# Performance work log

Hardware: AMD Instinct MI355X
Metric: run time of the kernel (lower is better)

Reference implementation:

```python
import jax, jax.numpy as jnp
import numpy as np

S, N, M, D, O = 16, 4096, 128, 128, 128


def setup_inputs() -> dict:
    key = jax.random.key(0)
    kF, kU, kmu, klp, keps = jax.random.split(key, 5)
    return {
        "F": jax.random.normal(kF, (S, N, D), jnp.float32),
        "U": jax.random.normal(kU, (S, M, D), jnp.float32),
        "pseud_mu": jax.random.normal(kmu, (O, M), jnp.float32),
        "pseud_logprec": 0.1 * jax.random.normal(klp, (O, M), jnp.float32),
        "eps": jax.random.normal(keps, (S, O, D), jnp.float32),
    }


def reference(F, U, pseud_mu, pseud_logprec, eps):
    # F: [S,N,D], U: [S,M,D], pseud_mu/pseud_logprec: [O,M], eps: [S,O,D]
    Dd = U.shape[-1]
    phiU = jax.nn.relu(U)                                   # [S,M,D]
    Lp = jnp.exp(pseud_logprec)                             # diag of pseudo precision, [O,M]
    # U^T diag(Lp) U and U^T diag(Lp) v, fused (no dense [M,M] diag, no [S,O,D,M] temp)
    UTLU = jnp.einsum("smd,om,sme->sode", phiU, Lp, phiU)   # [S,O,D,D]
    UTLv = jnp.einsum("smd,om->sod", phiU, Lp * pseud_mu)   # [S,O,D]
    # prior precision = exp(-logvar_p) = I (logvar_p is a fixed zero buffer)
    q_prec = UTLU + jnp.eye(Dd, dtype=UTLU.dtype)           # [S,O,D,D]
    Lc = jnp.linalg.cholesky(q_prec)                        # [S,O,D,D]
    eye = jnp.broadcast_to(jnp.eye(Dd, dtype=q_prec.dtype), q_prec.shape)
    Linv = jax.scipy.linalg.solve_triangular(Lc, eye, lower=True)
    # cholesky_inverse: q_cov = (L L^T)^{-1} = L^{-T} L^{-1}
    q_cov = jnp.einsum("soki,sokj->soij", Linv, Linv)       # [S,O,D,D]
    q_mu = jnp.einsum("sode,soe->sod", q_cov, UTLv)         # [S,O,D]
    # MVN rsample: w = mu + chol(cov) @ eps
    Lcov = jnp.linalg.cholesky(q_cov)                       # [S,O,D,D]
    w = q_mu + jnp.einsum("sode,soe->sod", Lcov, eps)       # [S,O,D]
    # KL(q || N(0, I)) per (s,o), summed over output dim -> [S]
    logdet_cov = 2.0 * jnp.sum(jnp.log(jnp.diagonal(Lcov, axis1=-2, axis2=-1)), axis=-1)
    tr_cov = jnp.trace(q_cov, axis1=-2, axis2=-1)
    kl = 0.5 * (tr_cov + jnp.sum(q_mu * q_mu, axis=-1) - Dd - logdet_cov)  # [S,O]
    kl = jnp.sum(kl, axis=-1)                               # [S]
    F_out = jnp.einsum("sod,snd->sno", w, jax.nn.relu(F))   # [S,N,O]
    U_out = jnp.einsum("sod,smd->smo", w, phiU)             # [S,M,O]
    return F_out, U_out, kl
```

## Files before the change

### kernel.cpp

```cpp
#include <hip/hip_runtime.h>

typedef unsigned int uint;
typedef unsigned short ushort;
typedef __attribute__((ext_vector_type(8))) short b16x8;
typedef __attribute__((ext_vector_type(4))) float f32x4;

#define PHIUT_OFF 0u
#define SQLP_OFF  524288u
#define SMU_OFF   (524288u + 65536u)
#define WBUF_OFF  (524288u + 131072u)
#define KLSO_OFF  (524288u + 131072u + 1048576u)

__device__ __forceinline__ ushort f2bf(float x){
  union { float f; uint u; } v; v.f = x;
  uint r = v.u + 0x7fffu + ((v.u >> 16) & 1u);
  return (ushort)(r >> 16);
}
__device__ __forceinline__ float bflo(uint u){ union { uint uu; float f; } v; v.uu = u << 16; return v.f; }
__device__ __forceinline__ float bfhi(uint u){ union { uint uu; float f; } v; v.uu = u & 0xffff0000u; return v.f; }
__device__ __forceinline__ uint pk2(float a, float b){ return (uint)f2bf(a) | ((uint)f2bf(b) << 16); }
__device__ __forceinline__ float rdl(float x, int l){
  union { float f; int i; } u; u.f = x;
  u.i = __builtin_amdgcn_readlane(u.i, l);
  return u.f;
}

__device__ __forceinline__ void mfma128(const ushort (*A)[136], const ushort (*B)[136],
                                        f32x4 acc[2][8], int wv, int lane){
  const int lr = lane & 15, lk = lane >> 4;
  #pragma unroll
  for (int ti = 0; ti < 2; ++ti)
    #pragma unroll
    for (int tj = 0; tj < 8; ++tj)
      acc[ti][tj] = (f32x4){0.f, 0.f, 0.f, 0.f};
  #pragma unroll
  for (int kk = 0; kk < 4; ++kk){
    const int kof = kk * 32 + lk * 8;
    b16x8 a0 = *(const b16x8*)&A[(wv * 2 + 0) * 16 + lr][kof];
    b16x8 a1 = *(const b16x8*)&A[(wv * 2 + 1) * 16 + lr][kof];
    #pragma unroll
    for (int tj = 0; tj < 8; ++tj){
      b16x8 bf = *(const b16x8*)&B[tj * 16 + lr][kof];
      acc[0][tj] = __builtin_amdgcn_mfma_f32_16x16x32_bf16(a0, bf, acc[0][tj], 0, 0, 0);
      acc[1][tj] = __builtin_amdgcn_mfma_f32_16x16x32_bf16(a1, bf, acc[1][tj], 0, 0, 0);
    }
  }
}

__global__ void k0_prep(const float* __restrict__ U, const float* __restrict__ mu,
                        const float* __restrict__ lp, ushort* __restrict__ phiUT,
                        float* __restrict__ sqlp, float* __restrict__ smu)
{
  __shared__ __align__(16) ushort T0[128][132];
  const int tid = threadIdx.x;
  const int bid = blockIdx.x;
  if (bid < 16){
    const float* Us = U + ((size_t)bid << 14);
    for (int e = tid * 4; e < 16384; e += 1024){
      f32x4 v = *(const f32x4*)&Us[e];
      int m = e >> 7, d = e & 127;
      uint2 pv; pv.x = pk2(fmaxf(v[0],0.f), fmaxf(v[1],0.f));
      pv.y = pk2(fmaxf(v[2],0.f), fmaxf(v[3],0.f));
      *(uint2*)&T0[m][d] = pv;
    }
    __syncthreads();
    ushort* op = phiUT + ((size_t)bid << 14);
    for (int e = tid; e < 16384; e += 256){
      int d = e >> 7, m2 = e & 127;
      op[e] = T0[m2][d];
    }
  } else {
    int idx = ((bid - 16) << 8) + tid;
    float l = lp[idx], m = mu[idx];
    float ex = expf(0.5f * l);
    sqlp[idx] = ex;
    smu[idx]  = ex * m;
  }
}

#define UPJ(J, T) { \
  float s0_=rdl(ya##J[0],(T)), s1_=rdl(ya##J[1],(T)), s2_=rdl(ya##J[2],(T)), s3_=rdl(ya##J[3],(T)); \
  ya##J[0] -= m0_*s0_; ya##J[1] -= m0_*s1_; ya##J[2] -= m0_*s2_; ya##J[3] -= m0_*s3_; \
  yb##J[0] -= m1_*s0_; yb##J[1] -= m1_*s1_; yb##J[2] -= m1_*s2_; yb##J[3] -= m1_*s3_; }

#define UPP0(P,T) { float s1_=rdl(ya##P[1],(T)), s2_=rdl(ya##P[2],(T)), s3_=rdl(ya##P[3],(T)); \
  ya##P[1]-=m0_*s1_; ya##P[2]-=m0_*s2_; ya##P[3]-=m0_*s3_; ya##P[0]=m0_; \
  yb##P[1]-=m1_*s1_; yb##P[2]-=m1_*s2_; yb##P[3]-=m1_*s3_; yb##P[0]=m1_; }
#define UPP1(P,T) { float s2_=rdl(ya##P[2],(T)), s3_=rdl(ya##P[3],(T)); \
  ya##P[2]-=m0_*s2_; ya##P[3]-=m0_*s3_; ya##P[1]=m0_; \
  yb##P[2]-=m1_*s2_; yb##P[3]-=m1_*s3_; yb##P[1]=m1_; }
#define UPP2(P,T) { float s3_=rdl(ya##P[3],(T)); \
  ya##P[3]-=m0_*s3_; ya##P[2]=m0_; \
  yb##P[3]-=m1_*s3_; yb##P[2]=m1_; }
#define UPP3(P,T) { ya##P[3]=m0_; yb##P[3]=m1_; }

#define TAIL7(T)
#define TAIL6(T) UPJ(7,T)
#define TAIL5(T) UPJ(6,T) TAIL6(T)
#define TAIL4(T) UPJ(5,T) TAIL5(T)
#define TAIL3(T) UPJ(4,T) TAIL4(T)
#define TAIL2(T) UPJ(3,T) TAIL3(T)
#define TAIL1(T) UPJ(2,T) TAIL2(T)
#define TAIL0(T) UPJ(1,T) TAIL1(T)

#define STEP(T, T4, TQ) { \
  float d_ = rdl(ya##T4[TQ], (T)); \
  if (lane == 0) dvec[k0 + (T)] = d_; \
  float rk_ = 1.0f / d_; \
  float m0_ = ya##T4[TQ] * rk_; \
  float m1_ = yb##T4[TQ] * rk_; \
  UPP##TQ(T4, T) \
  TAIL##T4(T) }

#define LD(J) ya##J = h0 ? *(f32x4*)&Bm[r0][k0 + 4*(J)] : z4; \
              yb##J = h1 ? *(f32x4*)&Bm[r1][k0 + 4*(J)] : z4;
#define ST(J) if (h0) *(f32x4*)&Bm[r0][k0 + 4*(J)] = ya##J; \
              if (h1) *(f32x4*)&Bm[r1][k0 + 4*(J)] = yb##J;

#define WPQ(ROW, Y0, Y1, Q) { \
  f32x4 d0_ = *(const f32x4*)&dvec[k0 + (Q)*8]; \
  f32x4 d1_ = *(const f32x4*)&dvec[k0 + (Q)*8 + 4]; \
  f32x4 a0_ = (f32x4){0.f,0.f,0.f,0.f} - Y0 * d0_; \
  f32x4 a1_ = (f32x4){0.f,0.f,0.f,0.f} - Y1 * d1_; \
  uint4 ua_, ub_; \
  ua_.x = pk2(a0_[0],a0_[1]); ua_.y = pk2(a0_[2],a0_[3]); \
  ua_.z = pk2(a1_[0],a1_[1]); ua_.w = pk2(a1_[2],a1_[3]); \
  ub_.x = pk2(Y0[0],Y0[1]);   ub_.y = pk2(Y0[2],Y0[3]); \
  ub_.z = pk2(Y1[0],Y1[1]);   ub_.w = pk2(Y1[2],Y1[3]); \
  int fidx_ = (ROW)*16 + (Q)*4; \
  *(uint4*)&Bm[fidx_ >> 6][68 + (fidx_ & 63)] = ua_; \
  *(uint4*)&Bm[32 + (fidx_ >> 6)][68 + (fidx_ & 63)] = ub_; }
#define WPROW(ROW, V0,V1,V2,V3,V4,V5,V6,V7) \
  WPQ(ROW, V0, V1, 0) WPQ(ROW, V2, V3, 1) WPQ(ROW, V4, V5, 2) WPQ(ROW, V6, V7, 3)

__global__ __launch_bounds__(256, 2) void k2_factor(
    const ushort* __restrict__ phiUT, const float* __restrict__ sqlp,
    const float* __restrict__ smu, const float* __restrict__ eps,
    float* __restrict__ wout, float* __restrict__ klso)
{
  __shared__ __align__(16) float Bm[128][132];
  __shared__ __align__(16) float Tscr[4][2][16][16];
  __shared__ __align__(16) float svec[128];
  __shared__ __align__(16) float smuv[128];
  __shared__ __align__(16) float epsv[128];
  __shared__ __align__(16) float utlv[128];
  __shared__ __align__(16) float dvec[128];
  __shared__ __align__(16) float pvec[128];
  __shared__ __align__(16) float qmuv[128];
  __shared__ __align__(16) float wtv[128];
  float* trv = smuv;
  float* red = svec;
  ushort (*Wt)[136] = (ushort (*)[136])&Bm[0][0];

  const int tid  = threadIdx.x;
  const int lane = tid & 63;
  const int wv   = tid >> 6;
  const int s    = blockIdx.x >> 7;
  const int o    = blockIdx.x & 127;

  if (tid < 128){
    svec[tid] = sqlp[(o << 7) + tid];
    epsv[tid] = eps[(((size_t)s * 128 + o) << 7) + 127 - tid];
  } else {
    int t2 = tid - 128;
    smuv[t2] = smu[(o << 7) + t2];
  }
  __syncthreads();

  for (int e = tid * 8; e < 16384; e += 2048){
    int dp = e >> 7, m = e & 127;
    const ushort* srcp = phiUT + (((size_t)s) << 14) + ((size_t)(127 - dp) << 7) + m;
    uint4 raw = *(const uint4*)srcp;
    f32x4 c0 = *(f32x4*)&svec[m];
    f32x4 c1 = *(f32x4*)&svec[m + 4];
    uint4 ov;
    ov.x = pk2(bflo(raw.x)*c0[0], bfhi(raw.x)*c0[1]);
    ov.y = pk2(bflo(raw.y)*c0[2], bfhi(raw.y)*c0[3]);
    ov.z = pk2(bflo(raw.z)*c1[0], bfhi(raw.z)*c1[1]);
    ov.w = pk2(bflo(raw.w)*c1[2], bfhi(raw.w)*c1[3]);
    *(uint4*)&Wt[dp][m] = ov;
  }
  __syncthreads();

  if (tid < 128){
    float acc3 = 0.f;
    for (int m = 0; m < 128; m += 8){
      uint4 raw = *(uint4*)&Wt[tid][m];
      f32x4 u0 = *(f32x4*)&smuv[m];
      f32x4 u1 = *(f32x4*)&smuv[m + 4];
      acc3 += bflo(raw.x) * u0[0] + bfhi(raw.x) * u0[1]
            + bflo(raw.y) * u0[2] + bfhi(raw.y) * u0[3]
            + bflo(raw.z) * u1[0] + bfhi(raw.z) * u1[1]
            + bflo(raw.w) * u1[2] + bfhi(raw.w) * u1[3];
    }
    utlv[tid] = acc3;
  }
  __syncthreads();

  f32x4 acc[2][8];
  mfma128(Wt, Wt, acc, wv, lane);
  __syncthreads();

  {
    const int lr = lane & 15, lk = lane >> 4;
    #pragma unroll
    for (int ti = 0; ti < 2; ++ti){
      #pragma unroll
      for (int tj = 0; tj < 8; ++tj){
        int c = tj * 16 + lr;
        #pragma unroll
        for (int q = 0; q < 4; ++q){
          int r = (wv * 2 + ti) * 16 + lk * 4 + q;
          float v = acc[ti][tj][q];
          if (r == c) v += 1.0f;
          Bm[r][c] = v;
        }
      }
    }
  }
  __syncthreads();

  for (int p = 0; p < 4; ++p){
    const int k0 = p << 5;
    const int nrows = 128 - k0;
    if (wv == 0){
      const int r0 = k0 + lane, r1 = k0 + 64 + lane;
      const bool h0 = lane < nrows;
      const bool h1 = (64 + lane) < nrows;
      const f32x4 z4 = (f32x4){0.f,0.f,0.f,0.f};
      f32x4 ya0,ya1,ya2,ya3,ya4,ya5,ya6,ya7;
      f32x4 yb0,yb1,yb2,yb3,yb4,yb5,yb6,yb7;
      LD(0) LD(1) LD(2) LD(3) LD(4) LD(5) LD(6) LD(7)

      STEP( 0,0,0) STEP( 1,0,1) STEP( 2,0,2) STEP( 3,0,3)
      STEP( 4,1,0) STEP( 5,1,1) STEP( 6,1,2) STEP( 7,1,3)
      STEP( 8,2,0) STEP( 9,2,1) STEP(10,2,2) STEP(11,2,3)
      STEP(12,3,0) STEP(13,3,1) STEP(14,3,2) STEP(15,3,3)
      STEP(16,4,0) STEP(17,4,1) STEP(18,4,2) STEP(19,4,3)
      STEP(20,5,0) STEP(21,5,1) STEP(22,5,2) STEP(23,5,3)
      STEP(24,6,0) STEP(25,6,1) STEP(26,6,2) STEP(27,6,3)
      STEP(28,7,0) STEP(29,7,1) STEP(30,7,2) STEP(31,7,3)

      ST(0) ST(1) ST(2) ST(3) ST(4) ST(5) ST(6) ST(7)
      if (lane < 32) Bm[r0][k0 + lane] = 1.0f;
      if (p < 3){
        if (h0 && lane >= 32) { WPROW(r0, ya0,ya1,ya2,ya3,ya4,ya5,ya6,ya7) }
        if (h1)               { WPROW(r1, yb0,yb1,yb2,yb3,yb4,yb5,yb6,yb7) }
      }
    }
    __syncthreads();
    if (p < 3){
      const int b0 = k0 + 32, n = 128 - b0, ntile = n >> 4;
      const int tiles = (ntile * (ntile + 1)) >> 1;
      const int nextra = ntile >> 1;
      const int ntot = tiles + nextra;
      const int lr = lane & 15, lk = lane >> 4;
      for (int idx = wv; idx < ntot; idx += 4){
        int i0, j0;
        if (idx >= tiles){
          int k = idx - tiles;
          i0 = b0 + (k << 5); j0 = i0 + 16;
        } else {
          int ti = 0;
          while ((ti + 1) * (ti + 2) / 2 <= idx) ++ti;
          int tj = idx - ti * (ti + 1) / 2;
          i0 = b0 + (ti << 4); j0 = b0 + (tj << 4);
        }
        int crow = i0 + (lk << 2), ccol = j0 + lr;
        f32x4 c;
        #pragma unroll
        for (int q = 0; q < 4; ++q) c[q] = Bm[crow + q][ccol];
        int pia = (i0 + lr) * 16 + (lk << 2);
        b16x8 af = *(const b16x8*)&Bm[pia >> 6][68 + (pia & 63)];
        int pib = (j0 + lr) * 16 + (lk << 2);
        b16x8 bfr = *(const b16x8*)&Bm[32 + (pib >> 6)][68 + (pib & 63)];
        c = __builtin_amdgcn_mfma_f32_16x16x32_bf16(af, bfr, c, 0, 0, 0);
        #pragma unroll
        for (int q = 0; q < 4; ++q) Bm[crow + q][ccol] = c[q];
      }
      __syncthreads();
    }
  }

  for (int e = tid; e < 2048; e += 256){
    int b = e >> 8, r = (e >> 4) & 15, c = e & 15;
    if (c > r) Bm[(b << 4) + r][(b << 4) + c] = 0.0f;
  }

  if (wv < 2){
    const int g = lane >> 4, c8 = lane & 15;
    const int ib = ((wv << 2) + g) << 4;
    float Lr[16], x[16];
    #pragma unroll
    for (int r = 0; r < 16; ++r){
      Lr[r] = Bm[ib + r][ib + c8];
      x[r] = (r == c8) ? 1.0f : 0.0f;
    }
    #pragma unroll
    for (int k = 0; k < 15; ++k){
      float xk = x[k];
      #pragma unroll
      for (int r = k + 1; r < 16; ++r){
        float lrk = __shfl(Lr[r], (lane & 48) | k);
        x[r] -= lrk * xk;
      }
    }
    #pragma unroll
    for (int r = 1; r < 16; ++r)
      if (r > c8) Bm[ib + r][ib + c8] = x[r];
  }
  __syncthreads();

  {
    const int xr = lane >> 2;
    const int xc = (lane & 3) << 2;
    for (int I = 1; I < 8; ++I){
      __syncthreads();
      for (int J = wv; J < I; J += 4){
        int slot = J >> 2;
        f32x4 tv = (f32x4){0.f, 0.f, 0.f, 0.f};
        for (int K = J; K < I; ++K){
          #pragma unroll
          for (int kk = 0; kk < 16; ++kk){
            float l = Bm[(I << 4) + xr][(K << 4) + kk];
            f32x4 srow = *(f32x4*)&Bm[(K << 4) + kk][(J << 4) + xc];
            tv += l * srow;
          }
        }
        *(f32x4*)&Tscr[wv][slot][xr][xc] = tv;
      }
      __syncthreads();
      for (int J = wv; J < I; J += 4){
        int slot = J >> 2;
        f32x4 x = *(f32x4*)&Tscr[wv][slot][xr][xc];
        for (int k = 0; k < xr; ++k){
          float sik = Bm[(I << 4) + xr][(I << 4) + k];
          x += sik * (*(f32x4*)&Tscr[wv][slot][k][xc]);
        }
        *(f32x4*)&Bm[(I << 4) + xr][(J << 4) + xc] = -x;
      }
    }
  }
  __syncthreads();

  if (tid < 128){
    int i = tid;
    float asq = 0.f, ap = 0.f;
    for (int j4 = 0; j4 <= (i >> 2); ++j4){
      f32x4 v = *(f32x4*)&Bm[i][j4 << 2];
      f32x4 uv = *(f32x4*)&utlv[j4 << 2];
      #pragma unroll
      for (int q = 0; q < 4; ++q){
        int j = (j4 << 2) + q;
        bool ok = (j <= i);
        float sv = ok ? v[q] : 0.f;
        asq += sv * sv;
        ap  += sv * (ok ? uv[q] : 0.f);
      }
    }
    pvec[i] = ap;
    trv[i] = asq / dvec[i];
  }
  __syncthreads();
  if (tid < 128){
    utlv[tid] = pvec[tid] / dvec[tid];
    epsv[tid] = epsv[tid] * rsqrtf(dvec[tid]);
  }
  __syncthreads();
  if (tid < 128){
    int j = tid;
    float aq = 0.f, aw = 0.f;
    for (int i = j; i < 128; ++i){
      float sij = Bm[i][j];
      aq += sij * utlv[i];
      aw += sij * epsv[i];
    }
    qmuv[j] = aq;
    wtv[j] = aq + aw;
  }
  __syncthreads();
  float ra = 0.f, rb = 0.f, rc = 0.f;
  if (tid < 128){
    ra = trv[tid];
    float q = qmuv[tid];
    rb = q * q;
    rc = logf(dvec[tid]);
  }
  #pragma unroll
  for (int off = 32; off > 0; off >>= 1){
    ra += __shfl_xor(ra, off);
    rb += __shfl_xor(rb, off);
    rc += __shfl_xor(rc, off);
  }
  if (lane == 0){
    red[wv * 4 + 0] = ra; red[wv * 4 + 1] = rb; red[wv * 4 + 2] = rc;
  }
  __syncthreads();
  if (tid == 0){
    float tr = red[0] + red[4] + red[8]  + red[12];
    float q2 = red[1] + red[5] + red[9]  + red[13];
    float ld = red[2] + red[6] + red[10] + red[14];
    klso[(s << 7) + o] = 0.5f * (tr + q2 - 128.0f + ld);
  }
  if (tid < 128)
    wout[(((size_t)(s << 7) + o) << 7) + tid] = wtv[127 - tid];
}

__global__ __launch_bounds__(256, 2) void k3_outs(
    const float* __restrict__ F, const float* __restrict__ U,
    const float* __restrict__ wbuf, float* __restrict__ out)
{
  __shared__ __align__(16) ushort Ab[128][136];
  __shared__ __align__(16) ushort Wb[128][136];
  const int tid = threadIdx.x;
  const int lane = tid & 63, wv = tid >> 6;
  const int bid = blockIdx.x;
  const float* src;
  float* dst;
  int s;
  if (bid < 512){
    s = bid >> 5;
    int t = bid & 31;
    size_t off = (((size_t)s * 4096) + (size_t)t * 128) * 128;
    src = F + off;
    dst = out + off;
  } else {
    s = bid - 512;
    src = U + ((size_t)s << 14);
    dst = out + (size_t)8388608 + ((size_t)s << 14);
  }
  for (int e = tid * 4; e < 16384; e += 1024){
    f32x4 v = *(const f32x4*)&src[e];
    uint2 pv; pv.x = pk2(fmaxf(v[0],0.f), fmaxf(v[1],0.f));
    pv.y = pk2(fmaxf(v[2],0.f), fmaxf(v[3],0.f));
    *(uint2*)&Ab[e >> 7][e & 127] = pv;
  }
  const float* wsrc = wbuf + ((size_t)s << 14);
  for (int e = tid * 4; e < 16384; e += 1024){
    f32x4 v = *(const f32x4*)&wsrc[e];
    uint2 pv; pv.x = pk2(v[0], v[1]); pv.y = pk2(v[2], v[3]);
    *(uint2*)&Wb[e >> 7][e & 127] = pv;
  }
  __syncthreads();
  f32x4 acc[2][8];
  mfma128(Ab, Wb, acc, wv, lane);
  const int lr = lane & 15, lk = lane >> 4;
  #pragma unroll
  for (int ti = 0; ti < 2; ++ti){
    #pragma unroll
    for (int tj = 0; tj < 8; ++tj){
      int c = tj * 16 + lr;
      #pragma unroll
      for (int q = 0; q < 4; ++q){
        int r = (wv * 2 + ti) * 16 + lk * 4 + q;
        dst[(size_t)r * 128 + c] = acc[ti][tj][q];
      }
    }
  }
}

__global__ void k4_klred(const float* __restrict__ klso, float* __restrict__ klout){
  __shared__ float sums[16][17];
  const int t = threadIdx.x;
  int s = t >> 4, ch = t & 15;
  float a = 0.f;
  for (int q = 0; q < 8; ++q) a += klso[(s << 7) + ch * 8 + q];
  sums[s][ch] = a;
  __syncthreads();
  if (t < 16){
    float r = 0.f;
    for (int c = 0; c < 16; ++c) r += sums[t][c];
    klout[t] = r;
  }
}

extern "C" void kernel_launch(void* const* d_in, const int* in_sizes, int n_in,
                              void* d_out, int out_size, void* d_ws, size_t ws_size,
                              hipStream_t stream) {
  const float* F   = (const float*)d_in[0];
  const float* U   = (const float*)d_in[1];
  const float* mu  = (const float*)d_in[2];
  const float* lp  = (const float*)d_in[3];
  const float* eps = (const float*)d_in[4];
  float* out = (float*)d_out;
  char* ws = (char*)d_ws;
  ushort* phiUT = (ushort*)(ws + PHIUT_OFF);
  float* sqlp = (float*)(ws + SQLP_OFF);
  float* smu  = (float*)(ws + SMU_OFF);
  float* wbuf = (float*)(ws + WBUF_OFF);
  float* klso = (float*)(ws + KLSO_OFF);

  k0_prep<<<dim3(80), dim3(256), 0, stream>>>(U, mu, lp, phiUT, sqlp, smu);
  k2_factor<<<dim3(2048), dim3(256), 0, stream>>>(phiUT, sqlp, smu, eps, wbuf, klso);
  k3_outs<<<dim3(528), dim3(256), 0, stream>>>(F, U, wbuf, out);
  k4_klred<<<dim3(1), dim3(256), 0, stream>>>(klso, out + 8650752);
}
```

Before: 450.4 us.

## Split serial per-row reductions across all 256 threads and vectorize block TRSM LDS reads

Three tid<128 phases (UTLv, trace/projection, and back-substitution for q_mu/w) now run on both halves of the 256-thread block. Each half covers half of the index range and the partial sums are combined through Tscr scratch. The blocked triangular-inverse update also switches from scalar LDS loads to float4 loads of the L row, processing four k terms at a time. The aim is to keep idle threads busy and cut LDS instruction count, at the cost of extra __syncthreads barriers and scratch traffic.

```diff
diff --git a/kernel.cpp b/kernel.cpp
--- a/kernel.cpp
+++ b/kernel.cpp
@@ -182,10 +182,14 @@
   }
   __syncthreads();
 
-  if (tid < 128){
+  {
+    float* sA = (float*)Tscr;
+    const int i3 = tid & 127, h3 = tid >> 7;
+    const int m0 = h3 << 6;
     float acc3 = 0.f;
-    for (int m = 0; m < 128; m += 8){
-      uint4 raw = *(uint4*)&Wt[tid][m];
+    #pragma unroll 4
+    for (int m = m0; m < m0 + 64; m += 8){
+      uint4 raw = *(uint4*)&Wt[i3][m];
       f32x4 u0 = *(f32x4*)&smuv[m];
       f32x4 u1 = *(f32x4*)&smuv[m + 4];
       acc3 += bflo(raw.x) * u0[0] + bfhi(raw.x) * u0[1]
@@ -193,8 +197,10 @@
             + bflo(raw.z) * u1[0] + bfhi(raw.z) * u1[1]
             + bflo(raw.w) * u1[2] + bfhi(raw.w) * u1[3];
     }
-    utlv[tid] = acc3;
-  }
+    sA[tid] = acc3;
+  }
+  __syncthreads();
+  if (tid < 128) utlv[tid] = ((float*)Tscr)[tid] + ((float*)Tscr)[tid + 128];
   __syncthreads();
 
   f32x4 acc[2][8];
@@ -314,17 +320,21 @@
   {
     const int xr = lane >> 2;
     const int xc = (lane & 3) << 2;
+    const f32x4 z4 = (f32x4){0.f,0.f,0.f,0.f};
     for (int I = 1; I < 8; ++I){
       __syncthreads();
       for (int J = wv; J < I; J += 4){
         int slot = J >> 2;
-        f32x4 tv = (f32x4){0.f, 0.f, 0.f, 0.f};
+        f32x4 tv = z4;
         for (int K = J; K < I; ++K){
           #pragma unroll
-          for (int kk = 0; kk < 16; ++kk){
-            float l = Bm[(I << 4) + xr][(K << 4) + kk];
-            f32x4 srow = *(f32x4*)&Bm[(K << 4) + kk][(J << 4) + xc];
-            tv += l * srow;
+          for (int t = 0; t < 4; ++t){
+            f32x4 lv = *(f32x4*)&Bm[(I << 4) + xr][(K << 4) + 4*t];
+            f32x4 s0 = *(f32x4*)&Bm[(K << 4) + 4*t + 0][(J << 4) + xc];
+            f32x4 s1 = *(f32x4*)&Bm[(K << 4) + 4*t + 1][(J << 4) + xc];
+            f32x4 s2 = *(f32x4*)&Bm[(K << 4) + 4*t + 2][(J << 4) + xc];
+            f32x4 s3 = *(f32x4*)&Bm[(K << 4) + 4*t + 3][(J << 4) + xc];
+            tv += lv[0]*s0 + lv[1]*s1 + lv[2]*s2 + lv[3]*s3;
           }
         }
         *(f32x4*)&Tscr[wv][slot][xr][xc] = tv;
@@ -332,10 +342,15 @@
       __syncthreads();
       for (int J = wv; J < I; J += 4){
         int slot = J >> 2;
-        f32x4 x = *(f32x4*)&Tscr[wv][slot][xr][xc];
-        for (int k = 0; k < xr; ++k){
-          float sik = Bm[(I << 4) + xr][(I << 4) + k];
-          x += sik * (*(f32x4*)&Tscr[wv][slot][k][xc]);
+        f32x4 x = z4;
+        #pragma unroll
+        for (int t = 0; t < 4; ++t){
+          f32x4 sv = *(f32x4*)&Bm[(I << 4) + xr][(I << 4) + 4*t];
+          f32x4 t0 = *(f32x4*)&Tscr[wv][slot][4*t + 0][xc];
+          f32x4 t1 = *(f32x4*)&Tscr[wv][slot][4*t + 1][xc];
+          f32x4 t2 = *(f32x4*)&Tscr[wv][slot][4*t + 2][xc];
+          f32x4 t3 = *(f32x4*)&Tscr[wv][slot][4*t + 3][xc];
+          x += sv[0]*t0 + sv[1]*t1 + sv[2]*t2 + sv[3]*t3;
         }
         *(f32x4*)&Bm[(I << 4) + xr][(J << 4) + xc] = -x;
       }
@@ -343,23 +358,35 @@
   }
   __syncthreads();
 
-  if (tid < 128){
-    int i = tid;
+  {
+    float* sA = (float*)Tscr;
+    float* sB = sA + 256;
+    const int i9 = tid & 127, h9 = tid >> 7;
+    const int n4 = i9 >> 2;
+    const int lo = h9 ? (n4 >> 1) + 1 : 0;
+    const int hi = h9 ? n4 : (n4 >> 1);
     float asq = 0.f, ap = 0.f;
-    for (int j4 = 0; j4 <= (i >> 2); ++j4){
-      f32x4 v = *(f32x4*)&Bm[i][j4 << 2];
+    #pragma unroll 4
+    for (int j4 = lo; j4 <= hi; ++j4){
+      f32x4 v = *(f32x4*)&Bm[i9][j4 << 2];
       f32x4 uv = *(f32x4*)&utlv[j4 << 2];
       #pragma unroll
       for (int q = 0; q < 4; ++q){
         int j = (j4 << 2) + q;
-        bool ok = (j <= i);
+        bool ok = (j <= i9);
         float sv = ok ? v[q] : 0.f;
         asq += sv * sv;
         ap  += sv * (ok ? uv[q] : 0.f);
       }
     }
-    pvec[i] = ap;
-    trv[i] = asq / dvec[i];
+    sA[tid] = asq; sB[tid] = ap;
+  }
+  __syncthreads();
+  if (tid < 128){
+    float* sA = (float*)Tscr;
+    float* sB = sA + 256;
+    pvec[tid] = sB[tid] + sB[tid + 128];
+    trv[tid]  = (sA[tid] + sA[tid + 128]) / dvec[tid];
   }
   __syncthreads();
   if (tid < 128){
@@ -367,16 +394,30 @@
     epsv[tid] = epsv[tid] * rsqrtf(dvec[tid]);
   }
   __syncthreads();
-  if (tid < 128){
-    int j = tid;
+  {
+    float* sA = (float*)Tscr;
+    float* sB = sA + 256;
+    const int j9 = tid & 127, h9 = tid >> 7;
+    const int mid = (j9 + 129) >> 1;
+    const int lo = h9 ? mid : j9;
+    const int hi = h9 ? 128 : mid;
     float aq = 0.f, aw = 0.f;
-    for (int i = j; i < 128; ++i){
-      float sij = Bm[i][j];
+    #pragma unroll 8
+    for (int i = lo; i < hi; ++i){
+      float sij = Bm[i][j9];
       aq += sij * utlv[i];
       aw += sij * epsv[i];
     }
-    qmuv[j] = aq;
-    wtv[j] = aq + aw;
+    sA[tid] = aq; sB[tid] = aw;
+  }
+  __syncthreads();
+  if (tid < 128){
+    float* sA = (float*)Tscr;
+    float* sB = sA + 256;
+    float aq = sA[tid] + sA[tid + 128];
+    float aw = sB[tid] + sB[tid + 128];
+    qmuv[tid] = aq;
+    wtv[tid] = aq + aw;
   }
   __syncthreads();
   float ra = 0.f, rb = 0.f, rc = 0.f;
```

Result: faster. 412.7 us (-8.4%).
